# Kernel tuning notes

Hardware: AMD Instinct MI355X
Metric: run time of the kernel (lower is better)

## Reference

```python
import jax, jax.numpy as jnp
import numpy as np

N_NODES = 50000
N_EDGES = 100000
NUM_RELS = 200
IN_DIM = 64
OUT_DIM = 64


def setup_inputs() -> dict:
    key = jax.random.key(0)
    k1, k2, k3, k4, k5, k6 = jax.random.split(key, 6)
    input_h = jax.random.normal(k1, (N_NODES, IN_DIM), dtype=jnp.float32)
    src = jax.random.randint(k2, (N_EDGES,), 0, N_NODES, dtype=jnp.int32)
    rel = jax.random.randint(k3, (N_EDGES,), 0, NUM_RELS, dtype=jnp.int32)
    dst = jax.random.randint(k4, (N_EDGES,), 0, N_NODES, dtype=jnp.int32)
    edges = jnp.stack([src, rel, dst], axis=1)  # (E, 3)
    # xavier_normal for relation weight: std = sqrt(2/(in+out))
    w_std = float(np.sqrt(2.0 / (IN_DIM + OUT_DIM)))
    weight = jax.random.normal(k5, (NUM_RELS, IN_DIM, OUT_DIM), dtype=jnp.float32) * w_std
    # xavier_uniform with leaky_relu(0.2) gain for self-loop weight
    gain = float(np.sqrt(2.0 / (1.0 + 0.2 ** 2)))
    bound = gain * float(np.sqrt(6.0 / (IN_DIM + OUT_DIM)))
    self_loop_weight = jax.random.uniform(
        k6, (IN_DIM, OUT_DIM), dtype=jnp.float32, minval=-bound, maxval=bound)
    return {"input_h": input_h, "edges": edges, "weight": weight,
            "self_loop_weight": self_loop_weight}


def reference(input_h, edges, weight, self_loop_weight):
    src, rel, dst = edges[:, 0], edges[:, 1], edges[:, 2]
    num_nodes = input_h.shape[0]
    num_edges = edges.shape[0]

    src_h = input_h[src]                      # (E, in) gather
    w_e = weight[rel]                         # (E, in, out) per-edge weight materialization
    msg = jnp.einsum('ei,eio->eo', src_h, w_e)  # per-edge bmm

    # torch quirk: index_matrix[dst] = arange(E) keeps the LAST write per dst,
    # so each edge's message is replaced by the message of the last edge
    # (in edge order) with the same destination.
    last_idx = jax.ops.segment_max(jnp.arange(num_edges, dtype=jnp.int32), dst,
                                   num_segments=num_nodes)  # (N,)
    msg = msg[last_idx[dst]]                  # (E, out)

    # scatter-mean aggregation by destination (nodes with no in-edges get 0)
    msg_sum = jax.ops.segment_sum(msg, dst, num_segments=num_nodes)          # (N, out)
    count = jax.ops.segment_sum(jnp.ones((num_edges,), msg.dtype), dst,
                                num_segments=num_nodes)                      # (N,)
    agg = jnp.where(count[:, None] > 0, msg_sum / jnp.maximum(count, 1.0)[:, None], 0.0)

    out = input_h @ self_loop_weight + agg    # self-loop plus aggregated messages
    return out
```

## Files before the change

kernel.cpp:

```cpp
#include <hip/hip_runtime.h>

#define N_NODES 50000
#define N_EDGES 100000
#define NUM_RELS 200
#define DIM 64
#define CAP 512
#define TILES 8
#define KPAD 72

typedef __attribute__((ext_vector_type(8))) short bf16x8;
typedef __attribute__((ext_vector_type(8))) unsigned short u16x8;
typedef __attribute__((ext_vector_type(4))) float f32x4;

#define OFF_LAST 0
#define OFF_CUR  50000
#define OFF_BN   50208
#define OFF_BS   152608
#define HB_OFF   1020032u
#define WT_OFF   7420032u

__device__ __forceinline__ unsigned short f2bf(float x) {
    union { float f; unsigned u; } v; v.f = x;
    unsigned r = v.u + 0x7FFFu + ((v.u >> 16) & 1u);
    return (unsigned short)(r >> 16);
}

#define T_EM 391
#define T_WT 201
#define T_HC 391

__global__ __launch_bounds__(256) void prep_kernel(
    const float* __restrict__ h, const float* __restrict__ weight,
    const float* __restrict__ wself, const int* __restrict__ edges,
    int* __restrict__ ws, unsigned short* __restrict__ hb,
    unsigned short* __restrict__ wt)
{
    __shared__ float Wl[DIM * DIM];
    int b = blockIdx.x, t = threadIdx.x;

    if (b < T_EM) {
        int e = b * 256 + t;
        if (e < N_EDGES) atomicMax(&ws[OFF_LAST + edges[e * 3 + 2]], e);
        return;
    }
    if (b < T_EM + T_WT) {
        int rel = b - T_EM;
        const float* src = (rel < NUM_RELS) ? (weight + (size_t)rel * DIM * DIM) : wself;
#pragma unroll
        for (int j = 0; j < 16; ++j) Wl[t + j * 256] = src[t + j * 256];
        __syncthreads();
        int cc = t >> 2, q = t & 3;
        unsigned short tmp[16];
#pragma unroll
        for (int kk = 0; kk < 16; ++kk)
            tmp[kk] = f2bf(Wl[(q * 16 + kk) * DIM + cc]);
        unsigned short* dst = wt + (size_t)rel * DIM * DIM + cc * DIM + q * 16;
        *(u16x8*)dst       = *(const u16x8*)&tmp[0];
        *(u16x8*)(dst + 8) = *(const u16x8*)&tmp[8];
        return;
    }
    {
        long off = (long)(b - T_EM - T_WT) * 8192 + (long)t * 32;
        if (off < (long)N_NODES * DIM) {
#pragma unroll
            for (int half = 0; half < 2; ++half) {
                const float4* src = (const float4*)(h + off + half * 16);
                unsigned short tmp[16];
#pragma unroll
                for (int j = 0; j < 4; ++j) {
                    float4 v = src[j];
                    tmp[j*4+0]=f2bf(v.x); tmp[j*4+1]=f2bf(v.y);
                    tmp[j*4+2]=f2bf(v.z); tmp[j*4+3]=f2bf(v.w);
                }
                *(u16x8*)(hb + off + half * 16)     = *(const u16x8*)&tmp[0];
                *(u16x8*)(hb + off + half * 16 + 8) = *(const u16x8*)&tmp[8];
            }
        }
    }
}

#define BK_BLKS 196
#define NODE_TILES 782

__global__ __launch_bounds__(256) void bucket_self_kernel(
    const int* __restrict__ edges, const unsigned short* __restrict__ hb,
    const unsigned short* __restrict__ wt, int* __restrict__ ws,
    float* __restrict__ out)
{
    __shared__ unsigned short Wsh[DIM * KPAD];
    __shared__ unsigned short Hs[DIM * KPAD];
    int t = threadIdx.x;

    if (blockIdx.x < BK_BLKS) {
        int n = blockIdx.x * 256 + t;
        if (n < N_NODES) {
            int li = ws[OFF_LAST + n];
            if (li >= 0) {
                int r = edges[li * 3 + 1];
                int s = edges[li * 3 + 0];
                int pos = atomicAdd(&ws[OFF_CUR + r], 1) + 1;
                if (pos < CAP) {
                    ws[OFF_BN + r * CAP + pos] = n;
                    ws[OFF_BS + r * CAP + pos] = s;
                }
            }
        }
        return;
    }

    int base = (blockIdx.x - BK_BLKS) * 64;
    int row = t >> 2, q = t & 3;
    {
        const unsigned short* wsrc = wt + (size_t)NUM_RELS * DIM * DIM + row * DIM + q * 16;
        *(u16x8*)&Wsh[row * KPAD + q * 16]     = *(const u16x8*)wsrc;
        *(u16x8*)&Wsh[row * KPAD + q * 16 + 8] = *(const u16x8*)(wsrc + 8);
        int n = base + row; if (n >= N_NODES) n = N_NODES - 1;
        const unsigned short* hsrc = hb + (size_t)n * DIM + q * 16;
        *(u16x8*)&Hs[row * KPAD + q * 16]     = *(const u16x8*)hsrc;
        *(u16x8*)&Hs[row * KPAD + q * 16 + 8] = *(const u16x8*)(hsrc + 8);
    }
    __syncthreads();

    int l = t & 63;
    int w = __builtin_amdgcn_readfirstlane(t >> 6);
    int r16 = l & 15, kb = l >> 4;

    bf16x8 a0 = *reinterpret_cast<const bf16x8*>(&Hs[(w * 16 + r16) * KPAD + kb * 8]);
    bf16x8 a1 = *reinterpret_cast<const bf16x8*>(&Hs[(w * 16 + r16) * KPAD + 32 + kb * 8]);

    int nn[4]; bool vv[4];
#pragma unroll
    for (int r = 0; r < 4; ++r) {
        nn[r] = base + w * 16 + kb * 4 + r;
        vv[r] = nn[r] < N_NODES;
    }

#pragma unroll
    for (int n4 = 0; n4 < 4; ++n4) {
        bf16x8 b0 = *reinterpret_cast<const bf16x8*>(&Wsh[(n4 * 16 + r16) * KPAD + kb * 8]);
        bf16x8 b1 = *reinterpret_cast<const bf16x8*>(&Wsh[(n4 * 16 + r16) * KPAD + 32 + kb * 8]);
        f32x4 acc = {0.f, 0.f, 0.f, 0.f};
        acc = __builtin_amdgcn_mfma_f32_16x16x32_bf16(a0, b0, acc, 0, 0, 0);
        acc = __builtin_amdgcn_mfma_f32_16x16x32_bf16(a1, b1, acc, 0, 0, 0);
#pragma unroll
        for (int r = 0; r < 4; ++r)
            if (vv[r]) out[(size_t)nn[r] * DIM + n4 * 16 + r16] = acc[r];
    }
}

__global__ __launch_bounds__(256) void msg_kernel(
    const unsigned short* __restrict__ hb, const unsigned short* __restrict__ wt,
    const int* __restrict__ ws, float* __restrict__ out)
{
    __shared__ unsigned short Wsh[DIM * KPAD];
    __shared__ unsigned short Hs[DIM * KPAD];

    int rel = blockIdx.x >> 3;
    int tile = blockIdx.x & 7;
    int c = ws[OFF_CUR + rel] + 1;
    if (c > CAP) c = CAP;
    int start = tile * 64;
    if (start >= c) return;

    int t = threadIdx.x;
    const int* bn = ws + OFF_BN + rel * CAP;
    const int* bs = ws + OFF_BS + rel * CAP;

    int row = t >> 2, q = t & 3;
    {
        const unsigned short* wsrc = wt + (size_t)rel * DIM * DIM + row * DIM + q * 16;
        *(u16x8*)&Wsh[row * KPAD + q * 16]     = *(const u16x8*)wsrc;
        *(u16x8*)&Wsh[row * KPAD + q * 16 + 8] = *(const u16x8*)(wsrc + 8);
        int pos = start + row; if (pos >= c) pos = c - 1;
        int s = bs[pos];
        const unsigned short* hsrc = hb + (size_t)s * DIM + q * 16;
        *(u16x8*)&Hs[row * KPAD + q * 16]     = *(const u16x8*)hsrc;
        *(u16x8*)&Hs[row * KPAD + q * 16 + 8] = *(const u16x8*)(hsrc + 8);
    }
    __syncthreads();

    int l = t & 63;
    int w = __builtin_amdgcn_readfirstlane(t >> 6);
    int r16 = l & 15, kb = l >> 4;

    bf16x8 a0 = *reinterpret_cast<const bf16x8*>(&Hs[(w * 16 + r16) * KPAD + kb * 8]);
    bf16x8 a1 = *reinterpret_cast<const bf16x8*>(&Hs[(w * 16 + r16) * KPAD + 32 + kb * 8]);

    int nn[4]; bool vv[4];
#pragma unroll
    for (int r = 0; r < 4; ++r) {
        int p = start + w * 16 + kb * 4 + r;
        vv[r] = p < c;
        nn[r] = bn[vv[r] ? p : 0];
    }

#pragma unroll
    for (int n4 = 0; n4 < 4; ++n4) {
        bf16x8 b0 = *reinterpret_cast<const bf16x8*>(&Wsh[(n4 * 16 + r16) * KPAD + kb * 8]);
        bf16x8 b1 = *reinterpret_cast<const bf16x8*>(&Wsh[(n4 * 16 + r16) * KPAD + 32 + kb * 8]);
        f32x4 acc = {0.f, 0.f, 0.f, 0.f};
        acc = __builtin_amdgcn_mfma_f32_16x16x32_bf16(a0, b0, acc, 0, 0, 0);
        acc = __builtin_amdgcn_mfma_f32_16x16x32_bf16(a1, b1, acc, 0, 0, 0);
#pragma unroll
        for (int r = 0; r < 4; ++r)
            if (vv[r]) out[(size_t)nn[r] * DIM + n4 * 16 + r16] += acc[r];
    }
}

extern "C" void kernel_launch(void* const* d_in, const int* in_sizes, int n_in,
                              void* d_out, int out_size, void* d_ws, size_t ws_size,
                              hipStream_t stream) {
    const float* h      = (const float*)d_in[0];
    const int*   edges  = (const int*)d_in[1];
    const float* weight = (const float*)d_in[2];
    const float* wself  = (const float*)d_in[3];
    float* out = (float*)d_out;
    int* wsi = (int*)d_ws;
    unsigned short* hb = (unsigned short*)((char*)d_ws + HB_OFF);
    unsigned short* wt = (unsigned short*)((char*)d_ws + WT_OFF);

    hipMemsetAsync(d_ws, 0xFF, (size_t)(N_NODES + 208) * 4, stream);

    prep_kernel<<<T_EM + T_WT + T_HC, 256, 0, stream>>>(h, weight, wself, edges, wsi, hb, wt);
    bucket_self_kernel<<<BK_BLKS + NODE_TILES, 256, 0, stream>>>(edges, hb, wt, wsi, out);
    msg_kernel<<<NUM_RELS * TILES, 256, 0, stream>>>(hb, wt, wsi, out);
}
```

Measured before the change: 62.76 us.

## Load MFMA A-operands directly from global and double rows per block

The self-loop and message GEMM blocks now read their A-fragments (bf16 node rows) straight from global memory into registers, with no LDS staging. Each block now covers 128 rows in two 64-row sub-tiles instead of 64, so the weight tile staged in LDS is reused twice and half as many blocks are launched. This cuts LDS traffic and weight reloads, and lets the A loads overlap the weight copy before the barrier. In exchange, global reads of A are less coalesced, each block has more work, and parallelism is lower.

```diff
diff --git a/kernel.cpp b/kernel.cpp
--- a/kernel.cpp
+++ b/kernel.cpp
@@ -5,7 +5,7 @@
 #define NUM_RELS 200
 #define DIM 64
 #define CAP 512
-#define TILES 8
+#define TILES 4
 #define KPAD 72
 
 typedef __attribute__((ext_vector_type(8))) short bf16x8;
@@ -80,7 +80,7 @@
 }
 
 #define BK_BLKS 196
-#define NODE_TILES 782
+#define SELF_TILES 391
 
 __global__ __launch_bounds__(256) void bucket_self_kernel(
     const int* __restrict__ edges, const unsigned short* __restrict__ hb,
@@ -88,7 +88,6 @@
     float* __restrict__ out)
 {
     __shared__ unsigned short Wsh[DIM * KPAD];
-    __shared__ unsigned short Hs[DIM * KPAD];
     int t = threadIdx.x;
 
     if (blockIdx.x < BK_BLKS) {
@@ -108,43 +107,47 @@
         return;
     }
 
-    int base = (blockIdx.x - BK_BLKS) * 64;
-    int row = t >> 2, q = t & 3;
+    int base = (blockIdx.x - BK_BLKS) * 128;
+    int l = t & 63;
+    int w = __builtin_amdgcn_readfirstlane(t >> 6);
+    int r16 = l & 15, kb = l >> 4;
+
+    int ar0 = base + w * 16 + r16;        if (ar0 >= N_NODES) ar0 = N_NODES - 1;
+    int ar1 = base + 64 + w * 16 + r16;   if (ar1 >= N_NODES) ar1 = N_NODES - 1;
+    const unsigned short* ap0 = hb + (size_t)ar0 * DIM + kb * 8;
+    const unsigned short* ap1 = hb + (size_t)ar1 * DIM + kb * 8;
+    bf16x8 a0 = *(const bf16x8*)ap0;
+    bf16x8 a1 = *(const bf16x8*)(ap0 + 32);
+    bf16x8 a2 = *(const bf16x8*)ap1;
+    bf16x8 a3 = *(const bf16x8*)(ap1 + 32);
+
     {
+        int row = t >> 2, q = t & 3;
         const unsigned short* wsrc = wt + (size_t)NUM_RELS * DIM * DIM + row * DIM + q * 16;
         *(u16x8*)&Wsh[row * KPAD + q * 16]     = *(const u16x8*)wsrc;
         *(u16x8*)&Wsh[row * KPAD + q * 16 + 8] = *(const u16x8*)(wsrc + 8);
-        int n = base + row; if (n >= N_NODES) n = N_NODES - 1;
-        const unsigned short* hsrc = hb + (size_t)n * DIM + q * 16;
-        *(u16x8*)&Hs[row * KPAD + q * 16]     = *(const u16x8*)hsrc;
-        *(u16x8*)&Hs[row * KPAD + q * 16 + 8] = *(const u16x8*)(hsrc + 8);
     }
     __syncthreads();
 
-    int l = t & 63;
-    int w = __builtin_amdgcn_readfirstlane(t >> 6);
-    int r16 = l & 15, kb = l >> 4;
-
-    bf16x8 a0 = *reinterpret_cast<const bf16x8*>(&Hs[(w * 16 + r16) * KPAD + kb * 8]);
-    bf16x8 a1 = *reinterpret_cast<const bf16x8*>(&Hs[(w * 16 + r16) * KPAD + 32 + kb * 8]);
-
-    int nn[4]; bool vv[4];
-#pragma unroll
-    for (int r = 0; r < 4; ++r) {
-        nn[r] = base + w * 16 + kb * 4 + r;
-        vv[r] = nn[r] < N_NODES;
-    }
-
-#pragma unroll
-    for (int n4 = 0; n4 < 4; ++n4) {
-        bf16x8 b0 = *reinterpret_cast<const bf16x8*>(&Wsh[(n4 * 16 + r16) * KPAD + kb * 8]);
-        bf16x8 b1 = *reinterpret_cast<const bf16x8*>(&Wsh[(n4 * 16 + r16) * KPAD + 32 + kb * 8]);
-        f32x4 acc = {0.f, 0.f, 0.f, 0.f};
-        acc = __builtin_amdgcn_mfma_f32_16x16x32_bf16(a0, b0, acc, 0, 0, 0);
-        acc = __builtin_amdgcn_mfma_f32_16x16x32_bf16(a1, b1, acc, 0, 0, 0);
-#pragma unroll
-        for (int r = 0; r < 4; ++r)
-            if (vv[r]) out[(size_t)nn[r] * DIM + n4 * 16 + r16] = acc[r];
+#pragma unroll
+    for (int sub = 0; sub < 2; ++sub) {
+        bf16x8 aa0 = sub ? a2 : a0;
+        bf16x8 aa1 = sub ? a3 : a1;
+        int sbase = base + sub * 64;
+        if (sbase >= N_NODES) break;
+#pragma unroll
+        for (int n4 = 0; n4 < 4; ++n4) {
+            bf16x8 b0 = *(const bf16x8*)&Wsh[(n4 * 16 + r16) * KPAD + kb * 8];
+            bf16x8 b1 = *(const bf16x8*)&Wsh[(n4 * 16 + r16) * KPAD + 32 + kb * 8];
+            f32x4 acc = {0.f, 0.f, 0.f, 0.f};
+            acc = __builtin_amdgcn_mfma_f32_16x16x32_bf16(aa0, b0, acc, 0, 0, 0);
+            acc = __builtin_amdgcn_mfma_f32_16x16x32_bf16(aa1, b1, acc, 0, 0, 0);
+#pragma unroll
+            for (int r = 0; r < 4; ++r) {
+                int nn = sbase + w * 16 + kb * 4 + r;
+                if (nn < N_NODES) out[(size_t)nn * DIM + n4 * 16 + r16] = acc[r];
+            }
+        }
     }
 }
 
@@ -153,57 +156,69 @@
     const int* __restrict__ ws, float* __restrict__ out)
 {
     __shared__ unsigned short Wsh[DIM * KPAD];
-    __shared__ unsigned short Hs[DIM * KPAD];
-
-    int rel = blockIdx.x >> 3;
-    int tile = blockIdx.x & 7;
+
+    int rel = blockIdx.x >> 2;
+    int tile = blockIdx.x & 3;
     int c = ws[OFF_CUR + rel] + 1;
     if (c > CAP) c = CAP;
-    int start = tile * 64;
+    int start = tile * 128;
     if (start >= c) return;
 
     int t = threadIdx.x;
+    int l = t & 63;
+    int w = __builtin_amdgcn_readfirstlane(t >> 6);
+    int r16 = l & 15, kb = l >> 4;
     const int* bn = ws + OFF_BN + rel * CAP;
     const int* bs = ws + OFF_BS + rel * CAP;
-
-    int row = t >> 2, q = t & 3;
+    bool has1 = (start + 64) < c;
+
+    int pa0 = start + w * 16 + r16; if (pa0 >= c) pa0 = c - 1;
+    int s0 = bs[pa0];
+    const unsigned short* ap0 = hb + (size_t)s0 * DIM + kb * 8;
+    bf16x8 a0 = *(const bf16x8*)ap0;
+    bf16x8 a1 = *(const bf16x8*)(ap0 + 32);
+
+    bf16x8 a2, a3;
+    if (has1) {
+        int pa1 = start + 64 + w * 16 + r16; if (pa1 >= c) pa1 = c - 1;
+        int s1 = bs[pa1];
+        const unsigned short* ap1 = hb + (size_t)s1 * DIM + kb * 8;
+        a2 = *(const bf16x8*)ap1;
+        a3 = *(const bf16x8*)(ap1 + 32);
+    }
+
     {
+        int row = t >> 2, q = t & 3;
         const unsigned short* wsrc = wt + (size_t)rel * DIM * DIM + row * DIM + q * 16;
         *(u16x8*)&Wsh[row * KPAD + q * 16]     = *(const u16x8*)wsrc;
         *(u16x8*)&Wsh[row * KPAD + q * 16 + 8] = *(const u16x8*)(wsrc + 8);
-        int pos = start + row; if (pos >= c) pos = c - 1;
-        int s = bs[pos];
-        const unsigned short* hsrc = hb + (size_t)s * DIM + q * 16;
-        *(u16x8*)&Hs[row * KPAD + q * 16]     = *(const u16x8*)hsrc;
-        *(u16x8*)&Hs[row * KPAD + q * 16 + 8] = *(const u16x8*)(hsrc + 8);
     }
     __syncthreads();
 
-    int l = t & 63;
-    int w = __builtin_amdgcn_readfirstlane(t >> 6);
-    int r16 = l & 15, kb = l >> 4;
-
-    bf16x8 a0 = *reinterpret_cast<const bf16x8*>(&Hs[(w * 16 + r16) * KPAD + kb * 8]);
-    bf16x8 a1 = *reinterpret_cast<const bf16x8*>(&Hs[(w * 16 + r16) * KPAD + 32 + kb * 8]);
-
-    int nn[4]; bool vv[4];
-#pragma unroll
-    for (int r = 0; r < 4; ++r) {
-        int p = start + w * 16 + kb * 4 + r;
-        vv[r] = p < c;
-        nn[r] = bn[vv[r] ? p : 0];
-    }
-
-#pragma unroll
-    for (int n4 = 0; n4 < 4; ++n4) {
-        bf16x8 b0 = *reinterpret_cast<const bf16x8*>(&Wsh[(n4 * 16 + r16) * KPAD + kb * 8]);
-        bf16x8 b1 = *reinterpret_cast<const bf16x8*>(&Wsh[(n4 * 16 + r16) * KPAD + 32 + kb * 8]);
-        f32x4 acc = {0.f, 0.f, 0.f, 0.f};
-        acc = __builtin_amdgcn_mfma_f32_16x16x32_bf16(a0, b0, acc, 0, 0, 0);
-        acc = __builtin_amdgcn_mfma_f32_16x16x32_bf16(a1, b1, acc, 0, 0, 0);
-#pragma unroll
-        for (int r = 0; r < 4; ++r)
-            if (vv[r]) out[(size_t)nn[r] * DIM + n4 * 16 + r16] += acc[r];
+    int nsub = has1 ? 2 : 1;
+    for (int sub = 0; sub < nsub; ++sub) {
+        bf16x8 aa0 = sub ? a2 : a0;
+        bf16x8 aa1 = sub ? a3 : a1;
+        int sbase = start + sub * 64;
+
+        int nn[4]; bool vv[4];
+#pragma unroll
+        for (int r = 0; r < 4; ++r) {
+            int p = sbase + w * 16 + kb * 4 + r;
+            vv[r] = p < c;
+            nn[r] = bn[vv[r] ? p : 0];
+        }
+#pragma unroll
+        for (int n4 = 0; n4 < 4; ++n4) {
+            bf16x8 b0 = *(const bf16x8*)&Wsh[(n4 * 16 + r16) * KPAD + kb * 8];
+            bf16x8 b1 = *(const bf16x8*)&Wsh[(n4 * 16 + r16) * KPAD + 32 + kb * 8];
+            f32x4 acc = {0.f, 0.f, 0.f, 0.f};
+            acc = __builtin_amdgcn_mfma_f32_16x16x32_bf16(aa0, b0, acc, 0, 0, 0);
+            acc = __builtin_amdgcn_mfma_f32_16x16x32_bf16(aa1, b1, acc, 0, 0, 0);
+#pragma unroll
+            for (int r = 0; r < 4; ++r)
+                if (vv[r]) out[(size_t)nn[r] * DIM + n4 * 16 + r16] += acc[r];
+        }
     }
 }
 
@@ -222,6 +237,6 @@
     hipMemsetAsync(d_ws, 0xFF, (size_t)(N_NODES + 208) * 4, stream);
 
     prep_kernel<<<T_EM + T_WT + T_HC, 256, 0, stream>>>(h, weight, wself, edges, wsi, hb, wt);
-    bucket_self_kernel<<<BK_BLKS + NODE_TILES, 256, 0, stream>>>(edges, hb, wt, wsi, out);
+    bucket_self_kernel<<<BK_BLKS + SELF_TILES, 256, 0, stream>>>(edges, hb, wt, wsi, out);
     msg_kernel<<<NUM_RELS * TILES, 256, 0, stream>>>(hb, wt, wsi, out);
 }
```

New measurement: 65.62 us. 1.05x slower.

## Merge self-loop and message GEMMs into one kernel using atomic accumulation

Applied to the files above, without the earlier changes.

Output zeroing moves into the prep kernel. The bucketing step becomes its own small kernel. The self-loop GEMM and the per-relation message GEMM now run as two block ranges of a single kernel, and both accumulate into the output with atomicAdd. This removes the ordering dependency that forced the message GEMM to wait for the self-loop write, so both GEMMs can overlap, at the cost of float atomics on every output element and an extra zeroing pass over the output.

```diff
diff --git a/kernel.cpp b/kernel.cpp
--- a/kernel.cpp
+++ b/kernel.cpp
@@ -28,12 +28,13 @@
 #define T_EM 391
 #define T_WT 201
 #define T_HC 391
+#define T_ZO 196
 
 __global__ __launch_bounds__(256) void prep_kernel(
     const float* __restrict__ h, const float* __restrict__ weight,
     const float* __restrict__ wself, const int* __restrict__ edges,
     int* __restrict__ ws, unsigned short* __restrict__ hb,
-    unsigned short* __restrict__ wt)
+    unsigned short* __restrict__ wt, float* __restrict__ out)
 {
     __shared__ float Wl[DIM * DIM];
     int b = blockIdx.x, t = threadIdx.x;
@@ -59,7 +60,7 @@
         *(u16x8*)(dst + 8) = *(const u16x8*)&tmp[8];
         return;
     }
-    {
+    if (b < T_EM + T_WT + T_HC) {
         long off = (long)(b - T_EM - T_WT) * 8192 + (long)t * 32;
         if (off < (long)N_NODES * DIM) {
 #pragma unroll
@@ -76,134 +77,123 @@
                 *(u16x8*)(hb + off + half * 16 + 8) = *(const u16x8*)&tmp[8];
             }
         }
-    }
-}
-
-#define BK_BLKS 196
-#define NODE_TILES 782
-
-__global__ __launch_bounds__(256) void bucket_self_kernel(
-    const int* __restrict__ edges, const unsigned short* __restrict__ hb,
-    const unsigned short* __restrict__ wt, int* __restrict__ ws,
-    float* __restrict__ out)
-{
-    __shared__ unsigned short Wsh[DIM * KPAD];
-    __shared__ unsigned short Hs[DIM * KPAD];
-    int t = threadIdx.x;
-
-    if (blockIdx.x < BK_BLKS) {
-        int n = blockIdx.x * 256 + t;
-        if (n < N_NODES) {
-            int li = ws[OFF_LAST + n];
-            if (li >= 0) {
-                int r = edges[li * 3 + 1];
-                int s = edges[li * 3 + 0];
-                int pos = atomicAdd(&ws[OFF_CUR + r], 1) + 1;
-                if (pos < CAP) {
-                    ws[OFF_BN + r * CAP + pos] = n;
-                    ws[OFF_BS + r * CAP + pos] = s;
-                }
-            }
-        }
         return;
     }
-
-    int base = (blockIdx.x - BK_BLKS) * 64;
-    int row = t >> 2, q = t & 3;
     {
-        const unsigned short* wsrc = wt + (size_t)NUM_RELS * DIM * DIM + row * DIM + q * 16;
-        *(u16x8*)&Wsh[row * KPAD + q * 16]     = *(const u16x8*)wsrc;
-        *(u16x8*)&Wsh[row * KPAD + q * 16 + 8] = *(const u16x8*)(wsrc + 8);
-        int n = base + row; if (n >= N_NODES) n = N_NODES - 1;
-        const unsigned short* hsrc = hb + (size_t)n * DIM + q * 16;
-        *(u16x8*)&Hs[row * KPAD + q * 16]     = *(const u16x8*)hsrc;
-        *(u16x8*)&Hs[row * KPAD + q * 16 + 8] = *(const u16x8*)(hsrc + 8);
-    }
-    __syncthreads();
-
-    int l = t & 63;
-    int w = __builtin_amdgcn_readfirstlane(t >> 6);
-    int r16 = l & 15, kb = l >> 4;
-
-    bf16x8 a0 = *reinterpret_cast<const bf16x8*>(&Hs[(w * 16 + r16) * KPAD + kb * 8]);
-    bf16x8 a1 = *reinterpret_cast<const bf16x8*>(&Hs[(w * 16 + r16) * KPAD + 32 + kb * 8]);
-
-    int nn[4]; bool vv[4];
-#pragma unroll
-    for (int r = 0; r < 4; ++r) {
-        nn[r] = base + w * 16 + kb * 4 + r;
-        vv[r] = nn[r] < N_NODES;
-    }
-
-#pragma unroll
-    for (int n4 = 0; n4 < 4; ++n4) {
-        bf16x8 b0 = *reinterpret_cast<const bf16x8*>(&Wsh[(n4 * 16 + r16) * KPAD + kb * 8]);
-        bf16x8 b1 = *reinterpret_cast<const bf16x8*>(&Wsh[(n4 * 16 + r16) * KPAD + 32 + kb * 8]);
-        f32x4 acc = {0.f, 0.f, 0.f, 0.f};
-        acc = __builtin_amdgcn_mfma_f32_16x16x32_bf16(a0, b0, acc, 0, 0, 0);
-        acc = __builtin_amdgcn_mfma_f32_16x16x32_bf16(a1, b1, acc, 0, 0, 0);
-#pragma unroll
-        for (int r = 0; r < 4; ++r)
-            if (vv[r]) out[(size_t)nn[r] * DIM + n4 * 16 + r16] = acc[r];
-    }
-}
-
-__global__ __launch_bounds__(256) void msg_kernel(
+        long base4 = (long)(b - T_EM - T_WT - T_HC) * 4096 + t;
+        float4* o4 = (float4*)out;
+        const long tot4 = (long)N_NODES * DIM / 4;
+        float4 z = make_float4(0.f, 0.f, 0.f, 0.f);
+#pragma unroll
+        for (int j = 0; j < 16; ++j) {
+            long idx = base4 + (long)j * 256;
+            if (idx < tot4) o4[idx] = z;
+        }
+    }
+}
+
+__global__ __launch_bounds__(256) void bucket_kernel(const int* __restrict__ edges,
+                                                     int* __restrict__ ws) {
+    int n = blockIdx.x * 256 + threadIdx.x;
+    if (n >= N_NODES) return;
+    int li = ws[OFF_LAST + n];
+    if (li < 0) return;
+    int r = edges[li * 3 + 1];
+    int s = edges[li * 3 + 0];
+    int pos = atomicAdd(&ws[OFF_CUR + r], 1) + 1;
+    if (pos < CAP) {
+        ws[OFF_BN + r * CAP + pos] = n;
+        ws[OFF_BS + r * CAP + pos] = s;
+    }
+}
+
+#define MSG_BLKS (NUM_RELS * TILES)
+#define SELF_TILES 782
+
+__global__ __launch_bounds__(256) void gemm_kernel(
     const unsigned short* __restrict__ hb, const unsigned short* __restrict__ wt,
     const int* __restrict__ ws, float* __restrict__ out)
 {
     __shared__ unsigned short Wsh[DIM * KPAD];
     __shared__ unsigned short Hs[DIM * KPAD];
 
-    int rel = blockIdx.x >> 3;
-    int tile = blockIdx.x & 7;
-    int c = ws[OFF_CUR + rel] + 1;
-    if (c > CAP) c = CAP;
-    int start = tile * 64;
-    if (start >= c) return;
-
     int t = threadIdx.x;
-    const int* bn = ws + OFF_BN + rel * CAP;
-    const int* bs = ws + OFF_BS + rel * CAP;
-
-    int row = t >> 2, q = t & 3;
-    {
-        const unsigned short* wsrc = wt + (size_t)rel * DIM * DIM + row * DIM + q * 16;
-        *(u16x8*)&Wsh[row * KPAD + q * 16]     = *(const u16x8*)wsrc;
-        *(u16x8*)&Wsh[row * KPAD + q * 16 + 8] = *(const u16x8*)(wsrc + 8);
-        int pos = start + row; if (pos >= c) pos = c - 1;
-        int s = bs[pos];
-        const unsigned short* hsrc = hb + (size_t)s * DIM + q * 16;
-        *(u16x8*)&Hs[row * KPAD + q * 16]     = *(const u16x8*)hsrc;
-        *(u16x8*)&Hs[row * KPAD + q * 16 + 8] = *(const u16x8*)(hsrc + 8);
-    }
-    __syncthreads();
-
     int l = t & 63;
     int w = __builtin_amdgcn_readfirstlane(t >> 6);
     int r16 = l & 15, kb = l >> 4;
-
-    bf16x8 a0 = *reinterpret_cast<const bf16x8*>(&Hs[(w * 16 + r16) * KPAD + kb * 8]);
-    bf16x8 a1 = *reinterpret_cast<const bf16x8*>(&Hs[(w * 16 + r16) * KPAD + 32 + kb * 8]);
-
-    int nn[4]; bool vv[4];
-#pragma unroll
-    for (int r = 0; r < 4; ++r) {
-        int p = start + w * 16 + kb * 4 + r;
-        vv[r] = p < c;
-        nn[r] = bn[vv[r] ? p : 0];
-    }
-
-#pragma unroll
-    for (int n4 = 0; n4 < 4; ++n4) {
-        bf16x8 b0 = *reinterpret_cast<const bf16x8*>(&Wsh[(n4 * 16 + r16) * KPAD + kb * 8]);
-        bf16x8 b1 = *reinterpret_cast<const bf16x8*>(&Wsh[(n4 * 16 + r16) * KPAD + 32 + kb * 8]);
-        f32x4 acc = {0.f, 0.f, 0.f, 0.f};
-        acc = __builtin_amdgcn_mfma_f32_16x16x32_bf16(a0, b0, acc, 0, 0, 0);
-        acc = __builtin_amdgcn_mfma_f32_16x16x32_bf16(a1, b1, acc, 0, 0, 0);
-#pragma unroll
-        for (int r = 0; r < 4; ++r)
-            if (vv[r]) out[(size_t)nn[r] * DIM + n4 * 16 + r16] += acc[r];
+    int row = t >> 2, q = t & 3;
+
+    if (blockIdx.x < MSG_BLKS) {
+        int rel = blockIdx.x >> 3, tile = blockIdx.x & 7;
+        int c = ws[OFF_CUR + rel] + 1;
+        if (c > CAP) c = CAP;
+        int start = tile * 64;
+        if (start >= c) return;
+
+        const int* bn = ws + OFF_BN + rel * CAP;
+        const int* bs = ws + OFF_BS + rel * CAP;
+        {
+            const unsigned short* wsrc = wt + (size_t)rel * DIM * DIM + row * DIM + q * 16;
+            *(u16x8*)&Wsh[row * KPAD + q * 16]     = *(const u16x8*)wsrc;
+            *(u16x8*)&Wsh[row * KPAD + q * 16 + 8] = *(const u16x8*)(wsrc + 8);
+            int pos = start + row; if (pos >= c) pos = c - 1;
+            int s = bs[pos];
+            const unsigned short* hsrc = hb + (size_t)s * DIM + q * 16;
+            *(u16x8*)&Hs[row * KPAD + q * 16]     = *(const u16x8*)hsrc;
+            *(u16x8*)&Hs[row * KPAD + q * 16 + 8] = *(const u16x8*)(hsrc + 8);
+        }
+        __syncthreads();
+
+        bf16x8 a0 = *(const bf16x8*)&Hs[(w * 16 + r16) * KPAD + kb * 8];
+        bf16x8 a1 = *(const bf16x8*)&Hs[(w * 16 + r16) * KPAD + 32 + kb * 8];
+
+        int nn[4]; bool vv[4];
+#pragma unroll
+        for (int r = 0; r < 4; ++r) {
+            int p = start + w * 16 + kb * 4 + r;
+            vv[r] = p < c;
+            nn[r] = bn[vv[r] ? p : 0];
+        }
+#pragma unroll
+        for (int n4 = 0; n4 < 4; ++n4) {
+            bf16x8 b0 = *(const bf16x8*)&Wsh[(n4 * 16 + r16) * KPAD + kb * 8];
+            bf16x8 b1 = *(const bf16x8*)&Wsh[(n4 * 16 + r16) * KPAD + 32 + kb * 8];
+            f32x4 acc = {0.f, 0.f, 0.f, 0.f};
+            acc = __builtin_amdgcn_mfma_f32_16x16x32_bf16(a0, b0, acc, 0, 0, 0);
+            acc = __builtin_amdgcn_mfma_f32_16x16x32_bf16(a1, b1, acc, 0, 0, 0);
+#pragma unroll
+            for (int r = 0; r < 4; ++r)
+                if (vv[r]) atomicAdd(&out[(size_t)nn[r] * DIM + n4 * 16 + r16], acc[r]);
+        }
+    } else {
+        int base = (blockIdx.x - MSG_BLKS) * 64;
+        {
+            const unsigned short* wsrc = wt + (size_t)NUM_RELS * DIM * DIM + row * DIM + q * 16;
+            *(u16x8*)&Wsh[row * KPAD + q * 16]     = *(const u16x8*)wsrc;
+            *(u16x8*)&Wsh[row * KPAD + q * 16 + 8] = *(const u16x8*)(wsrc + 8);
+            int n = base + row; if (n >= N_NODES) n = N_NODES - 1;
+            const unsigned short* hsrc = hb + (size_t)n * DIM + q * 16;
+            *(u16x8*)&Hs[row * KPAD + q * 16]     = *(const u16x8*)hsrc;
+            *(u16x8*)&Hs[row * KPAD + q * 16 + 8] = *(const u16x8*)(hsrc + 8);
+        }
+        __syncthreads();
+
+        bf16x8 a0 = *(const bf16x8*)&Hs[(w * 16 + r16) * KPAD + kb * 8];
+        bf16x8 a1 = *(const bf16x8*)&Hs[(w * 16 + r16) * KPAD + 32 + kb * 8];
+
+#pragma unroll
+        for (int n4 = 0; n4 < 4; ++n4) {
+            bf16x8 b0 = *(const bf16x8*)&Wsh[(n4 * 16 + r16) * KPAD + kb * 8];
+            bf16x8 b1 = *(const bf16x8*)&Wsh[(n4 * 16 + r16) * KPAD + 32 + kb * 8];
+            f32x4 acc = {0.f, 0.f, 0.f, 0.f};
+            acc = __builtin_amdgcn_mfma_f32_16x16x32_bf16(a0, b0, acc, 0, 0, 0);
+            acc = __builtin_amdgcn_mfma_f32_16x16x32_bf16(a1, b1, acc, 0, 0, 0);
+#pragma unroll
+            for (int r = 0; r < 4; ++r) {
+                int nn = base + w * 16 + kb * 4 + r;
+                if (nn < N_NODES) atomicAdd(&out[(size_t)nn * DIM + n4 * 16 + r16], acc[r]);
+            }
+        }
     }
 }
 
@@ -221,7 +211,8 @@
 
     hipMemsetAsync(d_ws, 0xFF, (size_t)(N_NODES + 208) * 4, stream);
 
-    prep_kernel<<<T_EM + T_WT + T_HC, 256, 0, stream>>>(h, weight, wself, edges, wsi, hb, wt);
-    bucket_self_kernel<<<BK_BLKS + NODE_TILES, 256, 0, stream>>>(edges, hb, wt, wsi, out);
-    msg_kernel<<<NUM_RELS * TILES, 256, 0, stream>>>(hb, wt, wsi, out);
-}
+    prep_kernel<<<T_EM + T_WT + T_HC + T_ZO, 256, 0, stream>>>(h, weight, wself, edges,
+                                                               wsi, hb, wt, out);
+    bucket_kernel<<<(N_NODES + 255) / 256, 256, 0, stream>>>(edges, wsi);
+    gemm_kernel<<<MSG_BLKS + SELF_TILES, 256, 0, stream>>>(hb, wt, wsi, out);
+}
```

Measured after the change: 69.96 us. 1.11x slower.
